# Optimization experiments

Measured on AMD Instinct MI355X. Metric: run time of the kernel, lower is better.

The kernel has to match this reference:

```python
import jax, jax.numpy as jnp
import numpy as np

NUM_OUT_POINTS = 8192  # init kwarg num_out_points


def setup_inputs() -> dict:
    key = jax.random.key(0)
    B, C, N = 32, 64, 65536
    x = jax.random.normal(key, (B, C, N), dtype=jnp.float32)
    return {"x": x}


def reference(x):
    # x: [B, C, N]. For each batch element draw a random permutation of the
    # N points and keep the first NUM_OUT_POINTS indices, then gather.
    B, C, N = x.shape
    keys = jax.random.split(jax.random.key(1), B)
    # idx: [B, K] int32, each row a prefix of an independent permutation of N
    idx = jax.vmap(lambda k: jax.random.permutation(k, N)[:NUM_OUT_POINTS])(keys)
    idx = idx.astype(jnp.int32)
    # gather along point axis: y[b, c, k] = x[b, c, idx[b, k]]
    y = jnp.take_along_axis(x, idx[:, None, :].astype(jnp.int64), axis=2)
    return y
```

## Files before the change

### kernel.cpp

```cpp
#include <hip/hip_runtime.h>
#include <stdint.h>

#define B_SZ 32
#define C_SZ 64
#define N_SZ 65536
#define K_SZ 8192
#define JCAP 80

__device__ __forceinline__ uint32_t rotl32(uint32_t v, int r) {
  return (v << r) | (v >> (32 - r));
}

__device__ __forceinline__ void threefry2x32(uint32_t k0, uint32_t k1,
                                             uint32_t x0, uint32_t x1,
                                             uint32_t& o0, uint32_t& o1) {
  const uint32_t ks2 = k0 ^ k1 ^ 0x1BD11BDAu;
  x0 += k0; x1 += k1;
#define TF_R(r) { x0 += x1; x1 = rotl32(x1, (r)); x1 ^= x0; }
  TF_R(13) TF_R(15) TF_R(26) TF_R(6)   x0 += k1;  x1 += ks2 + 1u;
  TF_R(17) TF_R(29) TF_R(16) TF_R(24)  x0 += ks2; x1 += k0  + 2u;
  TF_R(13) TF_R(15) TF_R(26) TF_R(6)   x0 += k0;  x1 += k1  + 3u;
  TF_R(17) TF_R(29) TF_R(16) TF_R(24)  x0 += k1;  x1 += ks2 + 4u;
  TF_R(13) TF_R(15) TF_R(26) TF_R(6)   x0 += ks2; x1 += k0  + 5u;
#undef TF_R
  o0 = x0; o1 = x1;
}

__device__ __forceinline__ void subkey_for_round(int b, int round,
                                                 uint32_t& sk0, uint32_t& sk1) {
  uint32_t c0, c1;
  threefry2x32(0u, 1u, 0u, (uint32_t)b, c0, c1);
  for (int r = 0; r < round; ++r) {
    uint32_t n0, n1;
    threefry2x32(c0, c1, 0u, 0u, n0, n1);
    c0 = n0; c1 = n1;
  }
  threefry2x32(c0, c1, 0u, 1u, sk0, sk1);
}

__global__ __launch_bounds__(256) void zero_small(uint32_t* __restrict__ hist,
                                                  uint32_t* __restrict__ jcnt) {
  const int b = blockIdx.x, t = threadIdx.x;
  hist[b * 256 + t] = 0;
  jcnt[b * 256 + t] = 0;
}

template <int ROUND>
__global__ __launch_bounds__(256) void gen_hist(uint64_t* __restrict__ A,
                                                uint32_t* __restrict__ hist) {
  __shared__ uint32_t h[256];
  const int t = threadIdx.x, blk = blockIdx.x, b = blockIdx.y;
  h[t] = 0; __syncthreads();
  uint32_t sk0, sk1;
  subkey_for_round(b, ROUND, sk0, sk1);
  uint64_t* __restrict__ dst = A + (size_t)b * N_SZ;
  const int base = blk * 4096;
#pragma unroll
  for (int e = 0; e < 16; ++e) {
    const int i = base + e * 256 + t;
    uint32_t o0, o1;
    threefry2x32(sk0, sk1, 0u, (uint32_t)i, o0, o1);
    const uint32_t bits = o0 ^ o1;
    dst[i] = ((uint64_t)bits << 16) | (uint64_t)i;
    atomicAdd(&h[bits >> 24], 1u);
  }
  __syncthreads();
  if (h[t]) atomicAdd(&hist[b * 256 + t], h[t]);
}

__global__ __launch_bounds__(256) void prefix_kernel(uint32_t* __restrict__ hist,
                                                     uint32_t* __restrict__ baseArr,
                                                     uint32_t* __restrict__ cur) {
  __shared__ uint32_t sc[256];
  const int b = blockIdx.x, d = threadIdx.x;
  const uint32_t h = hist[b * 256 + d];
  hist[b * 256 + d] = 0;
  sc[d] = h;
  __syncthreads();
  for (int off = 1; off < 256; off <<= 1) {
    const uint32_t y = (d >= off) ? sc[d - off] : 0u;
    __syncthreads();
    sc[d] += y;
    __syncthreads();
  }
  const uint32_t excl = sc[d] - h;
  baseArr[b * 257 + d] = excl;
  cur[b * 256 + d] = excl;
  if (d == 255) baseArr[b * 257 + 256] = sc[255];
}

__global__ __launch_bounds__(256) void scatter1(const uint64_t* __restrict__ A,
                                                uint64_t* __restrict__ BV,
                                                uint32_t* __restrict__ cur) {
  __shared__ uint32_t lcnt[256];
  __shared__ uint32_t gb[256];
  const int t = threadIdx.x, blk = blockIdx.x, b = blockIdx.y;
  lcnt[t] = 0; __syncthreads();
  const uint64_t* __restrict__ src = A + (size_t)b * N_SZ + blk * 4096;
  uint64_t v[16]; uint32_t r[16], dg[16];
#pragma unroll
  for (int e = 0; e < 16; ++e) {
    v[e] = src[e * 256 + t];
    dg[e] = (uint32_t)(v[e] >> 40) & 0xFFu;
    r[e] = atomicAdd(&lcnt[dg[e]], 1u);
  }
  __syncthreads();
  if (lcnt[t]) gb[t] = atomicAdd(&cur[b * 256 + t], lcnt[t]);
  __syncthreads();
  uint64_t* __restrict__ dst = BV + (size_t)b * N_SZ;
#pragma unroll
  for (int e = 0; e < 16; ++e)
    dst[gb[dg[e]] + r[e]] = v[e];
}

__global__ __launch_bounds__(256) void scatter2(const uint64_t* __restrict__ A,
                                                uint64_t* __restrict__ CV,
                                                uint32_t* __restrict__ cur,
                                                const uint32_t* __restrict__ baseArr) {
  __shared__ uint32_t lcnt[256];
  __shared__ uint32_t gb[256];
  __shared__ uint32_t keep[256];
  const int t = threadIdx.x, blk = blockIdx.x, b = blockIdx.y;
  lcnt[t] = 0;
  keep[t] = (baseArr[b * 257 + t] < K_SZ) ? 1u : 0u;
  __syncthreads();
  const uint64_t* __restrict__ src = A + (size_t)b * N_SZ + blk * 4096;
  uint64_t v[16]; uint32_t r[16], dg[16];
#pragma unroll
  for (int e = 0; e < 16; ++e) {
    v[e] = src[e * 256 + t];
    dg[e] = (uint32_t)(v[e] >> 40) & 0xFFu;
    r[e] = keep[dg[e]] ? atomicAdd(&lcnt[dg[e]], 1u) : 0u;
  }
  __syncthreads();
  if (lcnt[t]) gb[t] = atomicAdd(&cur[b * 256 + t], lcnt[t]);
  __syncthreads();
  uint64_t* __restrict__ dst = CV + (size_t)b * N_SZ;
#pragma unroll
  for (int e = 0; e < 16; ++e)
    if (keep[dg[e]]) dst[gb[dg[e]] + r[e]] = v[e];
}

__global__ __launch_bounds__(256) void rank_sort1(const uint64_t* __restrict__ BV,
                                                  const uint32_t* __restrict__ baseArr,
                                                  uint16_t* __restrict__ S1v) {
  __shared__ uint32_t sub[512];
  __shared__ uint16_t dg[512];
  __shared__ uint16_t idxt[512];
  __shared__ uint32_t hist[256];
  __shared__ uint32_t sc[256];
  __shared__ uint32_t cur[256];
  __shared__ uint32_t base2[257];
  const int t = threadIdx.x, u = blockIdx.x, b = blockIdx.y;
  const uint32_t base = baseArr[b * 257 + u];
  uint32_t n = baseArr[b * 257 + u + 1] - base;
  if (n > 512u) n = 512u;
  const uint64_t* __restrict__ g = BV + (size_t)b * N_SZ + base;

  hist[t] = 0; __syncthreads();
  uint64_t rec[2];
#pragma unroll
  for (int w = 0; w < 2; ++w) {
    const int e = t + w * 256;
    if (e < (int)n) {
      rec[w] = g[e];
      const uint32_t key = (uint32_t)(rec[w] >> 16);
      const uint32_t d = (key >> 16) & 0xFFu;
      sub[e] = ((key & 0xFFFFu) << 16) | (uint32_t)(rec[w] & 0xFFFFull);
      dg[e] = (uint16_t)d;
      atomicAdd(&hist[d], 1u);
    }
  }
  __syncthreads();
  sc[t] = hist[t]; __syncthreads();
  for (int off = 1; off < 256; off <<= 1) {
    const uint32_t y = (t >= off) ? sc[t - off] : 0u;
    __syncthreads();
    sc[t] += y;
    __syncthreads();
  }
  base2[t] = sc[t] - hist[t];
  cur[t] = sc[t] - hist[t];
  if (t == 255) base2[256] = sc[255];
  __syncthreads();
#pragma unroll
  for (int w = 0; w < 2; ++w) {
    const int e = t + w * 256;
    if (e < (int)n) idxt[atomicAdd(&cur[dg[e]], 1u)] = (uint16_t)e;
  }
  __syncthreads();
  uint16_t* __restrict__ out = S1v + (size_t)b * N_SZ + base;
#pragma unroll
  for (int w = 0; w < 2; ++w) {
    const int e = t + w * 256;
    if (e < (int)n) {
      const uint32_t d = dg[e], s = sub[e];
      const uint32_t lo = base2[d], hi = base2[d + 1];
      uint32_t r = 0;
      for (uint32_t i = lo; i < hi; ++i) r += (sub[idxt[i]] < s) ? 1u : 0u;
      out[d == 0 ? r : (lo + r)] = (uint16_t)(rec[w] & 0xFFFFull);
    }
  }
}

__global__ __launch_bounds__(256) void finalize_rank(const uint64_t* __restrict__ CV,
                                                     const uint32_t* __restrict__ baseArr,
                                                     const uint16_t* __restrict__ S1v,
                                                     uint32_t* __restrict__ jcnt,
                                                     uint32_t* __restrict__ jb) {
  __shared__ uint32_t sub[512];
  __shared__ uint16_t dg[512];
  __shared__ uint16_t idxt[512];
  __shared__ uint32_t hist[256];
  __shared__ uint32_t sc[256];
  __shared__ uint32_t cur[256];
  __shared__ uint32_t base2[257];
  const int t = threadIdx.x, u = blockIdx.x, b = blockIdx.y;
  const uint32_t base = baseArr[b * 257 + u];
  if (base >= K_SZ) return;
  uint32_t n = baseArr[b * 257 + u + 1] - base;
  if (n > 512u) n = 512u;
  const uint64_t* __restrict__ g = CV + (size_t)b * N_SZ + base;

  hist[t] = 0; __syncthreads();
  uint64_t rec[2];
#pragma unroll
  for (int w = 0; w < 2; ++w) {
    const int e = t + w * 256;
    if (e < (int)n) {
      rec[w] = g[e];
      const uint32_t key = (uint32_t)(rec[w] >> 16);
      const uint32_t d = (key >> 16) & 0xFFu;
      sub[e] = ((key & 0xFFFFu) << 16) | (uint32_t)(rec[w] & 0xFFFFull);
      dg[e] = (uint16_t)d;
      atomicAdd(&hist[d], 1u);
    }
  }
  __syncthreads();
  sc[t] = hist[t]; __syncthreads();
  for (int off = 1; off < 256; off <<= 1) {
    const uint32_t y = (t >= off) ? sc[t - off] : 0u;
    __syncthreads();
    sc[t] += y;
    __syncthreads();
  }
  base2[t] = sc[t] - hist[t];
  cur[t] = sc[t] - hist[t];
  if (t == 255) base2[256] = sc[255];
  __syncthreads();
#pragma unroll
  for (int w = 0; w < 2; ++w) {
    const int e = t + w * 256;
    if (e < (int)n) idxt[atomicAdd(&cur[dg[e]], 1u)] = (uint16_t)e;
  }
  __syncthreads();
  const uint16_t* __restrict__ s1 = S1v + (size_t)b * N_SZ;
#pragma unroll
  for (int w = 0; w < 2; ++w) {
    const int e = t + w * 256;
    if (e < (int)n) {
      const uint32_t d = dg[e], s = sub[e];
      const uint32_t lo = base2[d], hi = base2[d + 1];
      uint32_t r = 0;
      for (uint32_t i = lo; i < hi; ++i) r += (sub[idxt[i]] < s) ? 1u : 0u;
      const uint32_t q = base + lo + r;
      if (q < K_SZ) {
        const uint32_t p = (uint32_t)(rec[w] & 0xFFFFull);
        const uint32_t j = (uint32_t)s1[p];
        const uint32_t slot = atomicAdd(&jcnt[b * 256 + (j >> 8)], 1u);
        if (slot < JCAP)
          jb[((size_t)b * 256 + (j >> 8)) * JCAP + slot] = (j << 16) | q;
      }
    }
  }
}

__global__ __launch_bounds__(256) void compact_pairs(const uint32_t* __restrict__ jcnt,
                                                     const uint32_t* __restrict__ jb,
                                                     uint32_t* __restrict__ sp) {
  __shared__ uint32_t sc[256];
  __shared__ uint32_t cnt[256];
  const int b = blockIdx.x, t = threadIdx.x;
  uint32_t c = jcnt[b * 256 + t];
  if (c > JCAP) c = JCAP;
  cnt[t] = c; sc[t] = c;
  __syncthreads();
  for (int off = 1; off < 256; off <<= 1) {
    const uint32_t y = (t >= off) ? sc[t - off] : 0u;
    __syncthreads();
    sc[t] += y;
    __syncthreads();
  }
  const uint32_t base = sc[t] - cnt[t];
  const uint32_t* __restrict__ src = jb + ((size_t)b * 256 + t) * JCAP;
  uint32_t* __restrict__ dst = sp + (size_t)b * K_SZ + base;
  for (uint32_t i = 0; i < cnt[t]; ++i) dst[i] = src[i];
}

__global__ __launch_bounds__(256) void gather_staged(const float* __restrict__ x,
                                                     const uint32_t* __restrict__ sp,
                                                     float* __restrict__ y) {
  __shared__ float row[K_SZ];
  const int t = threadIdx.x, c = blockIdx.x, b = blockIdx.y;
  const uint32_t* __restrict__ spb = sp + (size_t)b * K_SZ;
  const float* __restrict__ xr = x + ((size_t)b * C_SZ + c) * N_SZ;
#pragma unroll 8
  for (int w = 0; w < 32; ++w) {
    const uint32_t p = spb[w * 256 + t];
    row[p & 0xFFFFu] = xr[p >> 16];
  }
  __syncthreads();
  float4* __restrict__ yr4 = (float4*)(y + ((size_t)b * C_SZ + c) * K_SZ);
  const float4* __restrict__ r4 = (const float4*)row;
#pragma unroll
  for (int w = 0; w < 8; ++w) yr4[w * 256 + t] = r4[w * 256 + t];
}

extern "C" void kernel_launch(void* const* d_in, const int* in_sizes, int n_in,
                              void* d_out, int out_size, void* d_ws, size_t ws_size,
                              hipStream_t stream) {
  (void)in_sizes; (void)n_in; (void)out_size; (void)ws_size;
  const float* x = (const float*)d_in[0];
  float* y = (float*)d_out;

  char* base = (char*)d_out;
  uint64_t* A  = (uint64_t*)base;
  uint64_t* BV = (uint64_t*)(base + (16u << 20));
  uint64_t* CV = (uint64_t*)(base + (32u << 20));
  uint32_t* hist    = (uint32_t*)(base + (48u << 20));
  uint32_t* baseArr = (uint32_t*)(base + (48u << 20) + (64u << 10));
  uint32_t* cur     = (uint32_t*)(base + (48u << 20) + (128u << 10));
  uint16_t* S1v     = (uint16_t*)(base + (52u << 20));
  uint32_t* jcnt = (uint32_t*)d_ws;
  uint32_t* jb   = (uint32_t*)((char*)d_ws + (64u << 10));
  uint32_t* sp   = (uint32_t*)((char*)d_ws + (4u << 20));

  const dim3 blk(256);
  const dim3 ggen(16, B_SZ);

  zero_small<<<dim3(B_SZ), blk, 0, stream>>>(hist, jcnt);
  gen_hist<0><<<ggen, blk, 0, stream>>>(A, hist);
  prefix_kernel<<<dim3(B_SZ), blk, 0, stream>>>(hist, baseArr, cur);
  scatter1<<<ggen, blk, 0, stream>>>(A, BV, cur);
  rank_sort1<<<dim3(256, B_SZ), blk, 0, stream>>>(BV, baseArr, S1v);
  gen_hist<1><<<ggen, blk, 0, stream>>>(A, hist);
  prefix_kernel<<<dim3(B_SZ), blk, 0, stream>>>(hist, baseArr, cur);
  scatter2<<<ggen, blk, 0, stream>>>(A, CV, cur, baseArr);
  finalize_rank<<<dim3(48, B_SZ), blk, 0, stream>>>(CV, baseArr, S1v, jcnt, jb);
  compact_pairs<<<dim3(B_SZ), blk, 0, stream>>>(jcnt, jb, sp);
  gather_staged<<<dim3(C_SZ, B_SZ), blk, 0, stream>>>(x, sp, y);
}
```

Baseline: 212.8 us.

## Fuse key generation with bucket scatter into fixed-capacity buckets

```diff
diff --git a/kernel.cpp b/kernel.cpp
--- a/kernel.cpp
+++ b/kernel.cpp
@@ -5,6 +5,8 @@
 #define C_SZ 64
 #define N_SZ 65536
 #define K_SZ 8192
+#define BCAP 384
+#define NHEAD 48
 #define JCAP 80
 
 __device__ __forceinline__ uint32_t rotl32(uint32_t v, int r) {
@@ -38,127 +40,77 @@
   threefry2x32(c0, c1, 0u, 1u, sk0, sk1);
 }
 
-__global__ __launch_bounds__(256) void zero_small(uint32_t* __restrict__ hist,
-                                                  uint32_t* __restrict__ jcnt) {
-  const int b = blockIdx.x, t = threadIdx.x;
-  hist[b * 256 + t] = 0;
-  jcnt[b * 256 + t] = 0;
-}
-
-template <int ROUND>
-__global__ __launch_bounds__(256) void gen_hist(uint64_t* __restrict__ A,
-                                                uint32_t* __restrict__ hist) {
-  __shared__ uint32_t h[256];
-  const int t = threadIdx.x, blk = blockIdx.x, b = blockIdx.y;
-  h[t] = 0; __syncthreads();
+__global__ __launch_bounds__(256) void zero_cnt(uint32_t* __restrict__ z) {
+  z[blockIdx.x * 256 + threadIdx.x] = 0;
+}
+
+__global__ __launch_bounds__(256) void gen_scatter1(uint64_t* __restrict__ BVfix,
+                                                    uint32_t* __restrict__ cnt1) {
+  __shared__ uint32_t lcnt[256];
+  __shared__ uint32_t gb[256];
+  const int t = threadIdx.x, chunk = blockIdx.x, b = blockIdx.y;
+  lcnt[t] = 0; __syncthreads();
   uint32_t sk0, sk1;
-  subkey_for_round(b, ROUND, sk0, sk1);
-  uint64_t* __restrict__ dst = A + (size_t)b * N_SZ;
-  const int base = blk * 4096;
+  subkey_for_round(b, 0, sk0, sk1);
+  uint64_t v[16]; uint32_t r[16], dg[16];
+  const int base = chunk * 4096;
 #pragma unroll
   for (int e = 0; e < 16; ++e) {
     const int i = base + e * 256 + t;
     uint32_t o0, o1;
     threefry2x32(sk0, sk1, 0u, (uint32_t)i, o0, o1);
     const uint32_t bits = o0 ^ o1;
-    dst[i] = ((uint64_t)bits << 16) | (uint64_t)i;
-    atomicAdd(&h[bits >> 24], 1u);
-  }
-  __syncthreads();
-  if (h[t]) atomicAdd(&hist[b * 256 + t], h[t]);
-}
-
-__global__ __launch_bounds__(256) void prefix_kernel(uint32_t* __restrict__ hist,
-                                                     uint32_t* __restrict__ baseArr,
-                                                     uint32_t* __restrict__ cur) {
+    v[e] = ((uint64_t)bits << 16) | (uint64_t)i;
+    dg[e] = bits >> 24;
+    r[e] = atomicAdd(&lcnt[dg[e]], 1u);
+  }
+  __syncthreads();
+  if (lcnt[t]) gb[t] = atomicAdd(&cnt1[b * 256 + t], lcnt[t]);
+  __syncthreads();
+#pragma unroll
+  for (int e = 0; e < 16; ++e) {
+    const uint32_t slot = gb[dg[e]] + r[e];
+    if (slot < BCAP)
+      BVfix[((size_t)(b * 256 + dg[e])) * BCAP + slot] = v[e];
+  }
+}
+
+__global__ __launch_bounds__(256) void prefix1(const uint32_t* __restrict__ cnt1,
+                                               uint32_t* __restrict__ baseArr) {
   __shared__ uint32_t sc[256];
   const int b = blockIdx.x, d = threadIdx.x;
-  const uint32_t h = hist[b * 256 + d];
-  hist[b * 256 + d] = 0;
-  sc[d] = h;
-  __syncthreads();
+  uint32_t h = cnt1[b * 256 + d];
+  if (h > BCAP) h = BCAP;
+  sc[d] = h; __syncthreads();
   for (int off = 1; off < 256; off <<= 1) {
     const uint32_t y = (d >= off) ? sc[d - off] : 0u;
     __syncthreads();
     sc[d] += y;
     __syncthreads();
   }
-  const uint32_t excl = sc[d] - h;
-  baseArr[b * 257 + d] = excl;
-  cur[b * 256 + d] = excl;
+  baseArr[b * 257 + d] = sc[d] - h;
   if (d == 255) baseArr[b * 257 + 256] = sc[255];
 }
 
-__global__ __launch_bounds__(256) void scatter1(const uint64_t* __restrict__ A,
-                                                uint64_t* __restrict__ BV,
-                                                uint32_t* __restrict__ cur) {
-  __shared__ uint32_t lcnt[256];
-  __shared__ uint32_t gb[256];
-  const int t = threadIdx.x, blk = blockIdx.x, b = blockIdx.y;
-  lcnt[t] = 0; __syncthreads();
-  const uint64_t* __restrict__ src = A + (size_t)b * N_SZ + blk * 4096;
-  uint64_t v[16]; uint32_t r[16], dg[16];
-#pragma unroll
-  for (int e = 0; e < 16; ++e) {
-    v[e] = src[e * 256 + t];
-    dg[e] = (uint32_t)(v[e] >> 40) & 0xFFu;
-    r[e] = atomicAdd(&lcnt[dg[e]], 1u);
-  }
-  __syncthreads();
-  if (lcnt[t]) gb[t] = atomicAdd(&cur[b * 256 + t], lcnt[t]);
-  __syncthreads();
-  uint64_t* __restrict__ dst = BV + (size_t)b * N_SZ;
-#pragma unroll
-  for (int e = 0; e < 16; ++e)
-    dst[gb[dg[e]] + r[e]] = v[e];
-}
-
-__global__ __launch_bounds__(256) void scatter2(const uint64_t* __restrict__ A,
-                                                uint64_t* __restrict__ CV,
-                                                uint32_t* __restrict__ cur,
-                                                const uint32_t* __restrict__ baseArr) {
-  __shared__ uint32_t lcnt[256];
-  __shared__ uint32_t gb[256];
-  __shared__ uint32_t keep[256];
-  const int t = threadIdx.x, blk = blockIdx.x, b = blockIdx.y;
-  lcnt[t] = 0;
-  keep[t] = (baseArr[b * 257 + t] < K_SZ) ? 1u : 0u;
-  __syncthreads();
-  const uint64_t* __restrict__ src = A + (size_t)b * N_SZ + blk * 4096;
-  uint64_t v[16]; uint32_t r[16], dg[16];
-#pragma unroll
-  for (int e = 0; e < 16; ++e) {
-    v[e] = src[e * 256 + t];
-    dg[e] = (uint32_t)(v[e] >> 40) & 0xFFu;
-    r[e] = keep[dg[e]] ? atomicAdd(&lcnt[dg[e]], 1u) : 0u;
-  }
-  __syncthreads();
-  if (lcnt[t]) gb[t] = atomicAdd(&cur[b * 256 + t], lcnt[t]);
-  __syncthreads();
-  uint64_t* __restrict__ dst = CV + (size_t)b * N_SZ;
-#pragma unroll
-  for (int e = 0; e < 16; ++e)
-    if (keep[dg[e]]) dst[gb[dg[e]] + r[e]] = v[e];
-}
-
-__global__ __launch_bounds__(256) void rank_sort1(const uint64_t* __restrict__ BV,
+__global__ __launch_bounds__(256) void rank_sort1(const uint64_t* __restrict__ BVfix,
+                                                  const uint32_t* __restrict__ cnt1,
                                                   const uint32_t* __restrict__ baseArr,
                                                   uint16_t* __restrict__ S1v) {
-  __shared__ uint32_t sub[512];
-  __shared__ uint16_t dg[512];
-  __shared__ uint16_t idxt[512];
+  __shared__ uint32_t sub[BCAP];
+  __shared__ uint16_t dg[BCAP];
+  __shared__ uint16_t idxt[BCAP];
   __shared__ uint32_t hist[256];
   __shared__ uint32_t sc[256];
   __shared__ uint32_t cur[256];
   __shared__ uint32_t base2[257];
   const int t = threadIdx.x, u = blockIdx.x, b = blockIdx.y;
+  uint32_t n = cnt1[b * 256 + u];
+  if (n > BCAP) n = BCAP;
+  const uint64_t* __restrict__ g = BVfix + ((size_t)(b * 256 + u)) * BCAP;
   const uint32_t base = baseArr[b * 257 + u];
-  uint32_t n = baseArr[b * 257 + u + 1] - base;
-  if (n > 512u) n = 512u;
-  const uint64_t* __restrict__ g = BV + (size_t)b * N_SZ + base;
 
   hist[t] = 0; __syncthreads();
-  uint64_t rec[2];
+  uint64_t rec[2] = {0, 0};
 #pragma unroll
   for (int w = 0; w < 2; ++w) {
     const int e = t + w * 256;
@@ -172,15 +124,16 @@
     }
   }
   __syncthreads();
-  sc[t] = hist[t]; __syncthreads();
+  const uint32_t h = hist[t];
+  sc[t] = h; __syncthreads();
   for (int off = 1; off < 256; off <<= 1) {
     const uint32_t y = (t >= off) ? sc[t - off] : 0u;
     __syncthreads();
     sc[t] += y;
     __syncthreads();
   }
-  base2[t] = sc[t] - hist[t];
-  cur[t] = sc[t] - hist[t];
+  base2[t] = sc[t] - h;
+  cur[t] = sc[t] - h;
   if (t == 255) base2[256] = sc[255];
   __syncthreads();
 #pragma unroll
@@ -189,7 +142,6 @@
     if (e < (int)n) idxt[atomicAdd(&cur[dg[e]], 1u)] = (uint16_t)e;
   }
   __syncthreads();
-  uint16_t* __restrict__ out = S1v + (size_t)b * N_SZ + base;
 #pragma unroll
   for (int w = 0; w < 2; ++w) {
     const int e = t + w * 256;
@@ -198,32 +150,82 @@
       const uint32_t lo = base2[d], hi = base2[d + 1];
       uint32_t r = 0;
       for (uint32_t i = lo; i < hi; ++i) r += (sub[idxt[i]] < s) ? 1u : 0u;
-      out[d == 0 ? r : (lo + r)] = (uint16_t)(rec[w] & 0xFFFFull);
-    }
-  }
-}
-
-__global__ __launch_bounds__(256) void finalize_rank(const uint64_t* __restrict__ CV,
-                                                     const uint32_t* __restrict__ baseArr,
+      S1v[(size_t)b * N_SZ + base + lo + r] = (uint16_t)(rec[w] & 0xFFFFull);
+    }
+  }
+}
+
+__global__ __launch_bounds__(256) void gen_scatter2(uint64_t* __restrict__ CVfix,
+                                                    uint32_t* __restrict__ cnt2) {
+  __shared__ uint32_t lcnt[256];
+  __shared__ uint32_t gb[256];
+  const int t = threadIdx.x, chunk = blockIdx.x, b = blockIdx.y;
+  lcnt[t] = 0; __syncthreads();
+  uint32_t sk0, sk1;
+  subkey_for_round(b, 1, sk0, sk1);
+  uint64_t v[16]; uint32_t r[16], dg[16];
+  const int base = chunk * 4096;
+#pragma unroll
+  for (int e = 0; e < 16; ++e) {
+    const int i = base + e * 256 + t;
+    uint32_t o0, o1;
+    threefry2x32(sk0, sk1, 0u, (uint32_t)i, o0, o1);
+    const uint32_t bits = o0 ^ o1;
+    v[e] = ((uint64_t)bits << 16) | (uint64_t)i;
+    dg[e] = bits >> 24;
+    r[e] = (dg[e] < NHEAD) ? atomicAdd(&lcnt[dg[e]], 1u) : 0u;
+  }
+  __syncthreads();
+  if (t < NHEAD && lcnt[t]) gb[t] = atomicAdd(&cnt2[b * 256 + t], lcnt[t]);
+  __syncthreads();
+#pragma unroll
+  for (int e = 0; e < 16; ++e) {
+    if (dg[e] < NHEAD) {
+      const uint32_t slot = gb[dg[e]] + r[e];
+      if (slot < BCAP)
+        CVfix[((size_t)(b * NHEAD + dg[e])) * BCAP + slot] = v[e];
+    }
+  }
+}
+
+__global__ __launch_bounds__(256) void prefix2(const uint32_t* __restrict__ cnt2,
+                                               uint32_t* __restrict__ baseArr2) {
+  __shared__ uint32_t sc[256];
+  const int b = blockIdx.x, d = threadIdx.x;
+  uint32_t h = 0;
+  if (d < NHEAD) { h = cnt2[b * 256 + d]; if (h > BCAP) h = BCAP; }
+  sc[d] = h; __syncthreads();
+  for (int off = 1; off < 256; off <<= 1) {
+    const uint32_t y = (d >= off) ? sc[d - off] : 0u;
+    __syncthreads();
+    sc[d] += y;
+    __syncthreads();
+  }
+  if (d < NHEAD) baseArr2[b * NHEAD + d] = sc[d] - h;
+}
+
+__global__ __launch_bounds__(256) void finalize_rank(const uint64_t* __restrict__ CVfix,
+                                                     const uint32_t* __restrict__ cnt2,
+                                                     const uint32_t* __restrict__ baseArr2,
                                                      const uint16_t* __restrict__ S1v,
                                                      uint32_t* __restrict__ jcnt,
                                                      uint32_t* __restrict__ jb) {
-  __shared__ uint32_t sub[512];
-  __shared__ uint16_t dg[512];
-  __shared__ uint16_t idxt[512];
+  __shared__ uint32_t sub[BCAP];
+  __shared__ uint16_t dg[BCAP];
+  __shared__ uint16_t idxt[BCAP];
   __shared__ uint32_t hist[256];
   __shared__ uint32_t sc[256];
   __shared__ uint32_t cur[256];
   __shared__ uint32_t base2[257];
   const int t = threadIdx.x, u = blockIdx.x, b = blockIdx.y;
-  const uint32_t base = baseArr[b * 257 + u];
+  const uint32_t base = baseArr2[b * NHEAD + u];
   if (base >= K_SZ) return;
-  uint32_t n = baseArr[b * 257 + u + 1] - base;
-  if (n > 512u) n = 512u;
-  const uint64_t* __restrict__ g = CV + (size_t)b * N_SZ + base;
+  uint32_t n = cnt2[b * 256 + u];
+  if (n > BCAP) n = BCAP;
+  const uint64_t* __restrict__ g = CVfix + ((size_t)(b * NHEAD + u)) * BCAP;
 
   hist[t] = 0; __syncthreads();
-  uint64_t rec[2];
+  uint64_t rec[2] = {0, 0};
 #pragma unroll
   for (int w = 0; w < 2; ++w) {
     const int e = t + w * 256;
@@ -237,15 +239,16 @@
     }
   }
   __syncthreads();
-  sc[t] = hist[t]; __syncthreads();
+  const uint32_t h = hist[t];
+  sc[t] = h; __syncthreads();
   for (int off = 1; off < 256; off <<= 1) {
     const uint32_t y = (t >= off) ? sc[t - off] : 0u;
     __syncthreads();
     sc[t] += y;
     __syncthreads();
   }
-  base2[t] = sc[t] - hist[t];
-  cur[t] = sc[t] - hist[t];
+  base2[t] = sc[t] - h;
+  cur[t] = sc[t] - h;
   if (t == 255) base2[256] = sc[255];
   __syncthreads();
 #pragma unroll
@@ -324,29 +327,27 @@
   float* y = (float*)d_out;
 
   char* base = (char*)d_out;
-  uint64_t* A  = (uint64_t*)base;
-  uint64_t* BV = (uint64_t*)(base + (16u << 20));
-  uint64_t* CV = (uint64_t*)(base + (32u << 20));
-  uint32_t* hist    = (uint32_t*)(base + (48u << 20));
-  uint32_t* baseArr = (uint32_t*)(base + (48u << 20) + (64u << 10));
-  uint32_t* cur     = (uint32_t*)(base + (48u << 20) + (128u << 10));
-  uint16_t* S1v     = (uint16_t*)(base + (52u << 20));
-  uint32_t* jcnt = (uint32_t*)d_ws;
-  uint32_t* jb   = (uint32_t*)((char*)d_ws + (64u << 10));
+  uint64_t* BVfix = (uint64_t*)base;
+  uint64_t* CVfix = (uint64_t*)(base + (26u << 20));
+  uint16_t* S1v   = (uint16_t*)(base + (31u << 20));
+  uint32_t* baseArr  = (uint32_t*)(base + (36u << 20));
+  uint32_t* baseArr2 = (uint32_t*)(base + (37u << 20));
+  uint32_t* cnt1 = (uint32_t*)d_ws;
+  uint32_t* cnt2 = (uint32_t*)((char*)d_ws + (32u << 10));
+  uint32_t* jcnt = (uint32_t*)((char*)d_ws + (64u << 10));
+  uint32_t* jb   = (uint32_t*)((char*)d_ws + (128u << 10));
   uint32_t* sp   = (uint32_t*)((char*)d_ws + (4u << 20));
 
   const dim3 blk(256);
   const dim3 ggen(16, B_SZ);
 
-  zero_small<<<dim3(B_SZ), blk, 0, stream>>>(hist, jcnt);
-  gen_hist<0><<<ggen, blk, 0, stream>>>(A, hist);
-  prefix_kernel<<<dim3(B_SZ), blk, 0, stream>>>(hist, baseArr, cur);
-  scatter1<<<ggen, blk, 0, stream>>>(A, BV, cur);
-  rank_sort1<<<dim3(256, B_SZ), blk, 0, stream>>>(BV, baseArr, S1v);
-  gen_hist<1><<<ggen, blk, 0, stream>>>(A, hist);
-  prefix_kernel<<<dim3(B_SZ), blk, 0, stream>>>(hist, baseArr, cur);
-  scatter2<<<ggen, blk, 0, stream>>>(A, CV, cur, baseArr);
-  finalize_rank<<<dim3(48, B_SZ), blk, 0, stream>>>(CV, baseArr, S1v, jcnt, jb);
+  zero_cnt<<<dim3(96), blk, 0, stream>>>(cnt1);
+  gen_scatter1<<<ggen, blk, 0, stream>>>(BVfix, cnt1);
+  prefix1<<<dim3(B_SZ), blk, 0, stream>>>(cnt1, baseArr);
+  rank_sort1<<<dim3(256, B_SZ), blk, 0, stream>>>(BVfix, cnt1, baseArr, S1v);
+  gen_scatter2<<<ggen, blk, 0, stream>>>(CVfix, cnt2);
+  prefix2<<<dim3(B_SZ), blk, 0, stream>>>(cnt2, baseArr2);
+  finalize_rank<<<dim3(NHEAD, B_SZ), blk, 0, stream>>>(CVfix, cnt2, baseArr2, S1v, jcnt, jb);
   compact_pairs<<<dim3(B_SZ), blk, 0, stream>>>(jcnt, jb, sp);
   gather_staged<<<dim3(C_SZ, B_SZ), blk, 0, stream>>>(x, sp, y);
 }
```

Measured after the change: 196.4 us. 7.7% less time.
